# Kernel optimization log

Measured on AMD Instinct MI355X. Metric: run time of the kernel, lower is better.

Reference implementation:

```python
import jax, jax.numpy as jnp
import numpy as np

B, S, D = 1, 4096, 2048
H, KV, HD = 16, 4, 128
GROUPS = H // KV
SCALE = HD ** -0.5
ROPE_BASE = 10000.0
NEG = -1e9


def _rope_tables():
    inv_freq = 1.0 / (ROPE_BASE ** (jnp.arange(0, HD, 2, dtype=jnp.float32) / HD))  # [HD/2]
    pos = jnp.arange(S, dtype=jnp.float32)
    freqs = pos[:, None] * inv_freq[None, :]            # [S, HD/2]
    emb = jnp.concatenate([freqs, freqs], axis=-1)      # [S, HD] (HF convention)
    return jnp.cos(emb)[None], jnp.sin(emb)[None]       # [1, S, HD]


def setup_inputs() -> dict:
    key = jax.random.key(0)
    ks = jax.random.split(key, 6)
    cos, sin = _rope_tables()
    causal = jnp.tril(jnp.ones((S, S), dtype=bool))
    attention_mask = jnp.where(causal, 0.0, NEG).astype(jnp.float32)[None, None]  # [1,1,S,S]
    std = 0.02
    return {
        "hidden_states": jax.random.normal(ks[0], (B, S, D), jnp.float32),
        "cos": cos.astype(jnp.float32),
        "sin": sin.astype(jnp.float32),
        "attention_mask": attention_mask,
        "wq": jax.random.normal(ks[1], (H * HD, D), jnp.float32) * std,
        "wk": jax.random.normal(ks[2], (KV * HD, D), jnp.float32) * std,
        "wv": jax.random.normal(ks[3], (KV * HD, D), jnp.float32) * std,
        "wo": jax.random.normal(ks[4], (D, H * HD), jnp.float32) * std,
    }


def _rotate_half(x):
    x1, x2 = x[..., : HD // 2], x[..., HD // 2:]
    return jnp.concatenate([-x2, x1], axis=-1)


def reference(hidden_states, cos, sin, attention_mask, wq, wk, wv, wo):
    b, s, _ = hidden_states.shape
    # projections -> [B, n_heads, S, HD]
    q = (hidden_states @ wq.T).reshape(b, s, H, HD).transpose(0, 2, 1, 3)
    k = (hidden_states @ wk.T).reshape(b, s, KV, HD).transpose(0, 2, 1, 3)
    v = (hidden_states @ wv.T).reshape(b, s, KV, HD).transpose(0, 2, 1, 3)
    # RoPE (HF apply_rotary_pos_emb, unsqueeze head dim)
    c, sn = cos[:, None], sin[:, None]
    q = q * c + _rotate_half(q) * sn
    k = k * c + _rotate_half(k) * sn
    # GQA: repeat kv heads
    k = jnp.repeat(k, GROUPS, axis=1)
    v = jnp.repeat(v, GROUPS, axis=1)
    # eager attention
    scores = jnp.einsum("bhqd,bhkd->bhqk", q, k) * SCALE + attention_mask
    attn = jax.nn.softmax(scores, axis=-1)
    out = jnp.einsum("bhqk,bhkd->bhqd", attn, v)
    out = out.transpose(0, 2, 1, 3).reshape(b, s, H * HD)
    # output projection (all-reduce is identity at world_size=1)
    return out @ wo.T
```

## Files before the change

### kernel.cpp

```cpp
#include <hip/hip_runtime.h>
#include <hip/hip_bf16.h>

#define SEQ   4096
#define DMODEL 2048
#define NHEAD 16
#define NKVH  4
#define HDIM  128
#define NQ    (NHEAD*HDIM)
#define NKV   (NKVH*HDIM)
#define NQKV  (NQ + 2*NKV)
#define SCALE 0.08838834764831845f
#define LOG2E 1.4426950408889634f
#define SCL2  (SCALE * LOG2E)

typedef __bf16 bf16x4 __attribute__((ext_vector_type(4)));
typedef __bf16 bf16x8 __attribute__((ext_vector_type(8)));
typedef float  f32x4  __attribute__((ext_vector_type(4)));

#define GLOBAL_CPTR(x) ((const __attribute__((address_space(1))) void*)(x))
#define LDS_PTR(x)     ((__attribute__((address_space(3))) void*)(x))

__global__ __launch_bounds__(256)
void convert_all(__bf16* __restrict__ wqkv, __bf16* __restrict__ wob,
                 __bf16* __restrict__ hb,
                 const float* __restrict__ wq, const float* __restrict__ wk,
                 const float* __restrict__ wv, const float* __restrict__ wo,
                 const float* __restrict__ hid)
{
    const int b = blockIdx.x;
    const float* src;
    __bf16* dst;
    int ib;
    if (b < 2048)      { src = wq;  dst = wqkv;                                 ib = b; }
    else if (b < 2560) { src = wk;  dst = wqkv + (size_t)NQ * DMODEL;           ib = b - 2048; }
    else if (b < 3072) { src = wv;  dst = wqkv + (size_t)(NQ + NKV) * DMODEL;   ib = b - 2560; }
    else if (b < 5120) { src = wo;  dst = wob;                                  ib = b - 3072; }
    else               { src = hid; dst = hb;                                   ib = b - 5120; }
    const size_t e0 = ((size_t)ib * 256 + threadIdx.x) * 8;
    const float4 a = *(const float4*)(src + e0);
    const float4 c = *(const float4*)(src + e0 + 4);
    bf16x8 o;
    o[0]=(__bf16)a.x; o[1]=(__bf16)a.y; o[2]=(__bf16)a.z; o[3]=(__bf16)a.w;
    o[4]=(__bf16)c.x; o[5]=(__bf16)c.y; o[6]=(__bf16)c.z; o[7]=(__bf16)c.w;
    *(bf16x8*)(dst + e0) = o;
}

__global__ __launch_bounds__(256)
void gemm_bt(const __bf16* __restrict__ A, const __bf16* __restrict__ Bw,
             void* __restrict__ Cv, __bf16* __restrict__ kb2, __bf16* __restrict__ vt2,
             const float* __restrict__ ct, const float* __restrict__ st,
             int M, int N, int K, int cmode)
{
    __shared__ alignas(16) __bf16 As[2][128*32];
    __shared__ alignas(16) __bf16 Bs[2][128*32];

    const int tid  = threadIdx.x;
    const int w    = tid >> 6;
    const int lane = tid & 63;
    const int l16  = lane & 15;
    const int quad = lane >> 4;
    const int m0 = blockIdx.y * 128;
    const int n0 = blockIdx.x * 128;

    const int srow = lane >> 2;
    const int scol = (((lane & 3) ^ ((lane >> 3) & 3)) * 8);
    const int rsw  = (quad ^ ((l16 >> 1) & 3)) * 8;

    const int wm = (w >> 1) * 64;
    int coff[4];
    #pragma unroll
    for (int nt = 0; nt < 4; ++nt)
        coff[nt] = (cmode == 3) ? ((w & 1) * 32 + ((nt & 2) ? 64 : 0) + (nt & 1) * 16)
                                : ((w & 1) * 64 + nt * 16);

    f32x4 acc[4][4];
    #pragma unroll
    for (int mt = 0; mt < 4; ++mt)
        #pragma unroll
        for (int nt = 0; nt < 4; ++nt)
            acc[mt][nt] = (f32x4){0.f, 0.f, 0.f, 0.f};

    auto STAGE = [&](int k0, int b) {
        #pragma unroll
        for (int c = 0; c < 2; ++c) {
            const int r0 = w * 32 + c * 16;
            const __bf16* ga = A + (size_t)(m0 + r0 + srow) * K + k0 + scol;
            __builtin_amdgcn_global_load_lds(GLOBAL_CPTR(ga), LDS_PTR(&As[b][r0 * 32]), 16, 0, 0);
            const __bf16* gb = Bw + (size_t)(n0 + r0 + srow) * K + k0 + scol;
            __builtin_amdgcn_global_load_lds(GLOBAL_CPTR(gb), LDS_PTR(&Bs[b][r0 * 32]), 16, 0, 0);
        }
    };

    STAGE(0, 0);
    for (int k0 = 0; k0 < K; k0 += 32) {
        const int b = (k0 >> 5) & 1;
        __syncthreads();
        if (k0 + 32 < K) STAGE(k0 + 32, b ^ 1);

        bf16x8 af[4], bf[4];
        #pragma unroll
        for (int mt = 0; mt < 4; ++mt)
            af[mt] = *(const bf16x8*)&As[b][(wm + mt*16 + l16) * 32 + rsw];
        #pragma unroll
        for (int nt = 0; nt < 4; ++nt)
            bf[nt] = *(const bf16x8*)&Bs[b][(coff[nt] + l16) * 32 + rsw];
        __builtin_amdgcn_s_setprio(1);
        #pragma unroll
        for (int mt = 0; mt < 4; ++mt)
            #pragma unroll
            for (int nt = 0; nt < 4; ++nt)
                acc[mt][nt] = __builtin_amdgcn_mfma_f32_16x16x32_bf16(
                    af[mt], bf[nt], acc[mt][nt], 0, 0, 0);
        __builtin_amdgcn_s_setprio(0);
    }

    if (cmode == 3) {
        if (n0 >= 2560) {
            #pragma unroll
            for (int mt = 0; mt < 4; ++mt)
                #pragma unroll
                for (int nt = 0; nt < 4; ++nt) {
                    const int col = (n0 - 2560) + coff[nt] + l16;
                    const int row = m0 + wm + mt*16 + quad*4;
                    bf16x4 pk;
                    #pragma unroll
                    for (int r = 0; r < 4; ++r) pk[r] = (__bf16)acc[mt][nt][r];
                    *(bf16x4*)&vt2[(size_t)col * M + row] = pk;
                }
        } else {
            __bf16* dst;
            int ncols, cb;
            if (n0 < 2048) { dst = (__bf16*)Cv; ncols = NQ;  cb = n0; }
            else           { dst = kb2;         ncols = NKV; cb = n0 - 2048; }
            #pragma unroll
            for (int mt = 0; mt < 4; ++mt)
                #pragma unroll
                for (int np = 0; np < 2; ++np) {
                    const int d = coff[np] + l16;
                    #pragma unroll
                    for (int r = 0; r < 4; ++r) {
                        const int s = m0 + wm + mt*16 + quad*4 + r;
                        const float c  = ct[s * HDIM + d];
                        const float sn = st[s * HDIM + d];
                        const float x1 = acc[mt][np][r];
                        const float x2 = acc[mt][np + 2][r];
                        dst[(size_t)s * ncols + cb + d]      = (__bf16)(x1 * c - x2 * sn);
                        dst[(size_t)s * ncols + cb + d + 64] = (__bf16)(x2 * c + x1 * sn);
                    }
                }
        }
    } else {
        float* Cf = (float*)Cv;
        #pragma unroll
        for (int mt = 0; mt < 4; ++mt)
            #pragma unroll
            for (int nt = 0; nt < 4; ++nt) {
                const int row = m0 + wm + mt*16 + quad*4;
                const int col = n0 + coff[nt] + l16;
                #pragma unroll
                for (int r = 0; r < 4; ++r)
                    Cf[(size_t)(row + r) * N + col] = acc[mt][nt][r];
            }
    }
}

__global__ __launch_bounds__(512, 4)
void attn_kernel(__bf16* __restrict__ QO, const __bf16* __restrict__ Kb,
                 const __bf16* __restrict__ Vt)
{
    __shared__ alignas(16) __bf16 Klds[2][4][64][32];
    __shared__ alignas(16) __bf16 Vlds[2][2][128][32];
    __shared__ alignas(16) __bf16 Ps[8][16][64];

    const int tid  = threadIdx.x;
    const int w    = tid >> 6;
    const int lane = tid & 63;
    const int l16  = lane & 15;
    const int quad = lane >> 4;
    const int bx = (int)blockIdx.x;
    const int h  = (int)blockIdx.y;
    const int g  = h >> 2;
    const int nbx = (int)gridDim.x;
    const int qt = (h < 8) ? (nbx - 1 - bx) : bx;
    const int m0 = qt * 128;
    const int wrow = m0 + w * 16;

    const int srow = lane >> 2;
    const int scol = (((lane & 3) ^ ((lane >> 3) & 3)) * 8);
    const int rsw  = (quad ^ ((l16 >> 1) & 3)) * 8;

    const int kcw = w & 3;
    const int hw  = w >> 2;

    bf16x8 qf[4];
    {
        const size_t qbase = (size_t)(wrow + l16) * NQ + h * HDIM;
        #pragma unroll
        for (int kc = 0; kc < 4; ++kc)
            qf[kc] = *(const bf16x8*)&QO[qbase + kc * 32 + quad * 8];
    }

    bf16x8 onesf;
    #pragma unroll
    for (int i = 0; i < 8; ++i) onesf[i] = (__bf16)1.0f;

    const __bf16* kSrc = Kb + (size_t)(hw * 32 + srow) * NKV + g * HDIM + kcw * 32 + scol;
    const __bf16* vSrc = Vt + (size_t)(g * HDIM + kcw * 32 + srow) * SEQ + hw * 32 + scol;

    auto STAGE = [&](int jj, int b) {
        const int n0g = jj * 64;
        #pragma unroll
        for (int c = 0; c < 2; ++c) {
            __builtin_amdgcn_global_load_lds(
                GLOBAL_CPTR(kSrc + (size_t)(n0g + c * 16) * NKV),
                LDS_PTR(&Klds[b][kcw][hw * 32 + c * 16][0]), 16, 0, 0);
            __builtin_amdgcn_global_load_lds(
                GLOBAL_CPTR(vSrc + (size_t)(c * 16) * SEQ + n0g),
                LDS_PTR(&Vlds[b][hw][kcw * 32 + c * 16][0]), 16, 0, 0);
        }
    };

    f32x4 lacc = (f32x4){0.f, 0.f, 0.f, 0.f};
    f32x4 oacc[8];
    #pragma unroll
    for (int t = 0; t < 8; ++t) oacc[t] = (f32x4){0.f, 0.f, 0.f, 0.f};

    const int njt = 2 * qt + 2;
    STAGE(0, 0);
    for (int j = 0; j < njt; ++j) {
        __syncthreads();
        if (j + 1 < njt) STAGE(j + 1, (j + 1) & 1);
        const int n0g = j * 64;
        if (n0g > wrow + 15) continue;
        const int b = j & 1;

        f32x4 sacc[4];
        #pragma unroll
        for (int nt = 0; nt < 4; ++nt) sacc[nt] = (f32x4){0.f, 0.f, 0.f, 0.f};
        __builtin_amdgcn_s_setprio(1);
        #pragma unroll
        for (int kc = 0; kc < 4; ++kc) {
            #pragma unroll
            for (int nt = 0; nt < 4; ++nt) {
                const bf16x8 kf = *(const bf16x8*)&Klds[b][kc][nt * 16 + l16][rsw];
                sacc[nt] = __builtin_amdgcn_mfma_f32_16x16x32_bf16(qf[kc], kf, sacc[nt], 0, 0, 0);
            }
        }
        __builtin_amdgcn_s_setprio(0);

        if (n0g + 64 > wrow) {
            #pragma unroll
            for (int r = 0; r < 4; ++r) {
                const int qr = wrow + quad * 4 + r;
                const int prow = quad * 4 + r;
                const int pxor = (prow & 7) << 3;
                #pragma unroll
                for (int nt = 0; nt < 4; ++nt) {
                    float e = exp2f(sacc[nt][r] * SCL2);
                    if ((n0g + nt * 16 + l16) > qr) e = 0.f;
                    Ps[w][prow][(nt * 16 + l16) ^ pxor] = (__bf16)e;
                }
            }
        } else {
            #pragma unroll
            for (int r = 0; r < 4; ++r) {
                const int prow = quad * 4 + r;
                const int pxor = (prow & 7) << 3;
                #pragma unroll
                for (int nt = 0; nt < 4; ++nt)
                    Ps[w][prow][(nt * 16 + l16) ^ pxor] = (__bf16)exp2f(sacc[nt][r] * SCL2);
            }
        }

        bf16x8 pa[2];
        #pragma unroll
        for (int kc = 0; kc < 2; ++kc)
            pa[kc] = *(const bf16x8*)&Ps[w][l16][(kc * 32 + quad * 8) ^ ((l16 & 7) << 3)];

        __builtin_amdgcn_s_setprio(1);
        lacc = __builtin_amdgcn_mfma_f32_16x16x32_bf16(pa[0], onesf, lacc, 0, 0, 0);
        lacc = __builtin_amdgcn_mfma_f32_16x16x32_bf16(pa[1], onesf, lacc, 0, 0, 0);
        #pragma unroll
        for (int kc = 0; kc < 2; ++kc)
            #pragma unroll
            for (int t = 0; t < 8; ++t) {
                const bf16x8 vf = *(const bf16x8*)&Vlds[b][kc][t * 16 + l16][rsw];
                oacc[t] = __builtin_amdgcn_mfma_f32_16x16x32_bf16(pa[kc], vf, oacc[t], 0, 0, 0);
            }
        __builtin_amdgcn_s_setprio(0);
    }

    float rinv[4];
    #pragma unroll
    for (int r = 0; r < 4; ++r) rinv[r] = 1.f / lacc[r];
    #pragma unroll
    for (int t = 0; t < 8; ++t)
        #pragma unroll
        for (int r = 0; r < 4; ++r) {
            const int qr = wrow + quad * 4 + r;
            QO[(size_t)qr * NQ + h * HDIM + t * 16 + l16] = (__bf16)(oacc[t][r] * rinv[r]);
        }
}

extern "C" void kernel_launch(void* const* d_in, const int* in_sizes, int n_in,
                              void* d_out, int out_size, void* d_ws, size_t ws_size,
                              hipStream_t stream)
{
    const float* hidden = (const float*)d_in[0];
    const float* cosp   = (const float*)d_in[1];
    const float* sinp   = (const float*)d_in[2];
    const float* wq = (const float*)d_in[4];
    const float* wk = (const float*)d_in[5];
    const float* wv = (const float*)d_in[6];
    const float* wo = (const float*)d_in[7];

    const size_t nw_q = (size_t)NQ  * DMODEL;
    const size_t nw_k = (size_t)NKV * DMODEL;
    const size_t nq_e = (size_t)SEQ * NQ;
    const size_t nk_e = (size_t)SEQ * NKV;

    __bf16* ws     = (__bf16*)d_ws;
    __bf16* wo_b   = ws;
    __bf16* wqkv_b = wo_b + nw_q;
    __bf16* qbuf   = wqkv_b + nw_q + 2 * nw_k;
    __bf16* kbuf   = qbuf + nq_e;
    __bf16* vtb    = kbuf + nk_e;
    __bf16* hbuf   = (__bf16*)d_out;

    convert_all<<<dim3(9216), dim3(256), 0, stream>>>(
        wqkv_b, wo_b, hbuf, wq, wk, wv, wo, hidden);

    gemm_bt<<<dim3(NQKV / 128, SEQ / 128), dim3(256), 0, stream>>>(
        hbuf, wqkv_b, qbuf, kbuf, vtb, cosp, sinp, SEQ, NQKV, DMODEL, 3);

    attn_kernel<<<dim3(SEQ / 128, NHEAD), dim3(512), 0, stream>>>(qbuf, kbuf, vtb);

    gemm_bt<<<dim3(DMODEL / 128, SEQ / 128), dim3(256), 0, stream>>>(
        qbuf, wo_b, d_out, nullptr, nullptr, nullptr, nullptr, SEQ, DMODEL, DMODEL, 1);
}
```

Baseline: 412.7 us.

## Give each attention wave two 16-row query tiles with 256-thread blocks

```diff
diff --git a/kernel.cpp b/kernel.cpp
--- a/kernel.cpp
+++ b/kernel.cpp
@@ -164,13 +164,13 @@
     }
 }
 
-__global__ __launch_bounds__(512, 4)
+__global__ __launch_bounds__(256, 2)
 void attn_kernel(__bf16* __restrict__ QO, const __bf16* __restrict__ Kb,
                  const __bf16* __restrict__ Vt)
 {
     __shared__ alignas(16) __bf16 Klds[2][4][64][32];
     __shared__ alignas(16) __bf16 Vlds[2][2][128][32];
-    __shared__ alignas(16) __bf16 Ps[8][16][64];
+    __shared__ alignas(16) __bf16 Ps[4][32][64];
 
     const int tid  = threadIdx.x;
     const int w    = tid >> 6;
@@ -183,47 +183,49 @@
     const int nbx = (int)gridDim.x;
     const int qt = (h < 8) ? (nbx - 1 - bx) : bx;
     const int m0 = qt * 128;
-    const int wrow = m0 + w * 16;
+    const int wrow = m0 + w * 32;
 
     const int srow = lane >> 2;
     const int scol = (((lane & 3) ^ ((lane >> 3) & 3)) * 8);
     const int rsw  = (quad ^ ((l16 >> 1) & 3)) * 8;
 
-    const int kcw = w & 3;
-    const int hw  = w >> 2;
-
-    bf16x8 qf[4];
-    {
-        const size_t qbase = (size_t)(wrow + l16) * NQ + h * HDIM;
+    bf16x8 qf[2][4];
+    #pragma unroll
+    for (int mt = 0; mt < 2; ++mt) {
+        const size_t qbase = (size_t)(wrow + mt * 16 + l16) * NQ + h * HDIM;
         #pragma unroll
         for (int kc = 0; kc < 4; ++kc)
-            qf[kc] = *(const bf16x8*)&QO[qbase + kc * 32 + quad * 8];
+            qf[mt][kc] = *(const bf16x8*)&QO[qbase + kc * 32 + quad * 8];
     }
 
     bf16x8 onesf;
     #pragma unroll
     for (int i = 0; i < 8; ++i) onesf[i] = (__bf16)1.0f;
 
-    const __bf16* kSrc = Kb + (size_t)(hw * 32 + srow) * NKV + g * HDIM + kcw * 32 + scol;
-    const __bf16* vSrc = Vt + (size_t)(g * HDIM + kcw * 32 + srow) * SEQ + hw * 32 + scol;
+    const __bf16* kSrc = Kb + (size_t)srow * NKV + g * HDIM + w * 32 + scol;
+    const __bf16* vSrc = Vt + (size_t)(g * HDIM + (w >> 1) * 64 + srow) * SEQ + (w & 1) * 32 + scol;
 
     auto STAGE = [&](int jj, int b) {
         const int n0g = jj * 64;
         #pragma unroll
-        for (int c = 0; c < 2; ++c) {
+        for (int c = 0; c < 4; ++c) {
             __builtin_amdgcn_global_load_lds(
                 GLOBAL_CPTR(kSrc + (size_t)(n0g + c * 16) * NKV),
-                LDS_PTR(&Klds[b][kcw][hw * 32 + c * 16][0]), 16, 0, 0);
+                LDS_PTR(&Klds[b][w][c * 16][0]), 16, 0, 0);
             __builtin_amdgcn_global_load_lds(
                 GLOBAL_CPTR(vSrc + (size_t)(c * 16) * SEQ + n0g),
-                LDS_PTR(&Vlds[b][hw][kcw * 32 + c * 16][0]), 16, 0, 0);
+                LDS_PTR(&Vlds[b][w & 1][(w >> 1) * 64 + c * 16][0]), 16, 0, 0);
         }
     };
 
-    f32x4 lacc = (f32x4){0.f, 0.f, 0.f, 0.f};
-    f32x4 oacc[8];
-    #pragma unroll
-    for (int t = 0; t < 8; ++t) oacc[t] = (f32x4){0.f, 0.f, 0.f, 0.f};
+    f32x4 lacc[2];
+    f32x4 oacc[2][8];
+    #pragma unroll
+    for (int mt = 0; mt < 2; ++mt) {
+        lacc[mt] = (f32x4){0.f, 0.f, 0.f, 0.f};
+        #pragma unroll
+        for (int t = 0; t < 8; ++t) oacc[mt][t] = (f32x4){0.f, 0.f, 0.f, 0.f};
+    }
 
     const int njt = 2 * qt + 2;
     STAGE(0, 0);
@@ -231,75 +233,91 @@
         __syncthreads();
         if (j + 1 < njt) STAGE(j + 1, (j + 1) & 1);
         const int n0g = j * 64;
-        if (n0g > wrow + 15) continue;
+        if (n0g > wrow + 31) continue;
         const int b = j & 1;
 
-        f32x4 sacc[4];
-        #pragma unroll
-        for (int nt = 0; nt < 4; ++nt) sacc[nt] = (f32x4){0.f, 0.f, 0.f, 0.f};
+        f32x4 sacc[2][4];
+        #pragma unroll
+        for (int mt = 0; mt < 2; ++mt)
+            #pragma unroll
+            for (int nt = 0; nt < 4; ++nt) sacc[mt][nt] = (f32x4){0.f, 0.f, 0.f, 0.f};
         __builtin_amdgcn_s_setprio(1);
         #pragma unroll
         for (int kc = 0; kc < 4; ++kc) {
             #pragma unroll
             for (int nt = 0; nt < 4; ++nt) {
                 const bf16x8 kf = *(const bf16x8*)&Klds[b][kc][nt * 16 + l16][rsw];
-                sacc[nt] = __builtin_amdgcn_mfma_f32_16x16x32_bf16(qf[kc], kf, sacc[nt], 0, 0, 0);
+                sacc[0][nt] = __builtin_amdgcn_mfma_f32_16x16x32_bf16(qf[0][kc], kf, sacc[0][nt], 0, 0, 0);
+                sacc[1][nt] = __builtin_amdgcn_mfma_f32_16x16x32_bf16(qf[1][kc], kf, sacc[1][nt], 0, 0, 0);
             }
         }
         __builtin_amdgcn_s_setprio(0);
 
-        if (n0g + 64 > wrow) {
-            #pragma unroll
-            for (int r = 0; r < 4; ++r) {
-                const int qr = wrow + quad * 4 + r;
-                const int prow = quad * 4 + r;
-                const int pxor = (prow & 7) << 3;
-                #pragma unroll
-                for (int nt = 0; nt < 4; ++nt) {
-                    float e = exp2f(sacc[nt][r] * SCL2);
-                    if ((n0g + nt * 16 + l16) > qr) e = 0.f;
-                    Ps[w][prow][(nt * 16 + l16) ^ pxor] = (__bf16)e;
+        #pragma unroll
+        for (int mt = 0; mt < 2; ++mt) {
+            const int rowbase = wrow + mt * 16;
+            if (n0g + 64 > rowbase) {
+                #pragma unroll
+                for (int r = 0; r < 4; ++r) {
+                    const int qr = rowbase + quad * 4 + r;
+                    const int prow = mt * 16 + quad * 4 + r;
+                    const int pxor = (prow & 7) << 3;
+                    #pragma unroll
+                    for (int nt = 0; nt < 4; ++nt) {
+                        float e = exp2f(sacc[mt][nt][r] * SCL2);
+                        if ((n0g + nt * 16 + l16) > qr) e = 0.f;
+                        Ps[w][prow][(nt * 16 + l16) ^ pxor] = (__bf16)e;
+                    }
                 }
-            }
-        } else {
-            #pragma unroll
-            for (int r = 0; r < 4; ++r) {
-                const int prow = quad * 4 + r;
-                const int pxor = (prow & 7) << 3;
-                #pragma unroll
-                for (int nt = 0; nt < 4; ++nt)
-                    Ps[w][prow][(nt * 16 + l16) ^ pxor] = (__bf16)exp2f(sacc[nt][r] * SCL2);
-            }
-        }
-
-        bf16x8 pa[2];
-        #pragma unroll
-        for (int kc = 0; kc < 2; ++kc)
-            pa[kc] = *(const bf16x8*)&Ps[w][l16][(kc * 32 + quad * 8) ^ ((l16 & 7) << 3)];
+            } else {
+                #pragma unroll
+                for (int r = 0; r < 4; ++r) {
+                    const int prow = mt * 16 + quad * 4 + r;
+                    const int pxor = (prow & 7) << 3;
+                    #pragma unroll
+                    for (int nt = 0; nt < 4; ++nt)
+                        Ps[w][prow][(nt * 16 + l16) ^ pxor] = (__bf16)exp2f(sacc[mt][nt][r] * SCL2);
+                }
+            }
+        }
+
+        bf16x8 pa[2][2];
+        #pragma unroll
+        for (int mt = 0; mt < 2; ++mt)
+            #pragma unroll
+            for (int kc = 0; kc < 2; ++kc)
+                pa[mt][kc] = *(const bf16x8*)&Ps[w][mt * 16 + l16][(kc * 32 + quad * 8) ^ ((l16 & 7) << 3)];
 
         __builtin_amdgcn_s_setprio(1);
-        lacc = __builtin_amdgcn_mfma_f32_16x16x32_bf16(pa[0], onesf, lacc, 0, 0, 0);
-        lacc = __builtin_amdgcn_mfma_f32_16x16x32_bf16(pa[1], onesf, lacc, 0, 0, 0);
+        #pragma unroll
+        for (int mt = 0; mt < 2; ++mt) {
+            lacc[mt] = __builtin_amdgcn_mfma_f32_16x16x32_bf16(pa[mt][0], onesf, lacc[mt], 0, 0, 0);
+            lacc[mt] = __builtin_amdgcn_mfma_f32_16x16x32_bf16(pa[mt][1], onesf, lacc[mt], 0, 0, 0);
+        }
         #pragma unroll
         for (int kc = 0; kc < 2; ++kc)
             #pragma unroll
             for (int t = 0; t < 8; ++t) {
                 const bf16x8 vf = *(const bf16x8*)&Vlds[b][kc][t * 16 + l16][rsw];
-                oacc[t] = __builtin_amdgcn_mfma_f32_16x16x32_bf16(pa[kc], vf, oacc[t], 0, 0, 0);
+                oacc[0][t] = __builtin_amdgcn_mfma_f32_16x16x32_bf16(pa[0][kc], vf, oacc[0][t], 0, 0, 0);
+                oacc[1][t] = __builtin_amdgcn_mfma_f32_16x16x32_bf16(pa[1][kc], vf, oacc[1][t], 0, 0, 0);
             }
         __builtin_amdgcn_s_setprio(0);
     }
 
-    float rinv[4];
-    #pragma unroll
-    for (int r = 0; r < 4; ++r) rinv[r] = 1.f / lacc[r];
-    #pragma unroll
-    for (int t = 0; t < 8; ++t)
-        #pragma unroll
-        for (int r = 0; r < 4; ++r) {
-            const int qr = wrow + quad * 4 + r;
-            QO[(size_t)qr * NQ + h * HDIM + t * 16 + l16] = (__bf16)(oacc[t][r] * rinv[r]);
-        }
+    #pragma unroll
+    for (int mt = 0; mt < 2; ++mt) {
+        float rinv[4];
+        #pragma unroll
+        for (int r = 0; r < 4; ++r) rinv[r] = 1.f / lacc[mt][r];
+        #pragma unroll
+        for (int t = 0; t < 8; ++t)
+            #pragma unroll
+            for (int r = 0; r < 4; ++r) {
+                const int qr = wrow + mt * 16 + quad * 4 + r;
+                QO[(size_t)qr * NQ + h * HDIM + t * 16 + l16] = (__bf16)(oacc[mt][t][r] * rinv[r]);
+            }
+    }
 }
 
 extern "C" void kernel_launch(void* const* d_in, const int* in_sizes, int n_in,
@@ -333,7 +351,7 @@
     gemm_bt<<<dim3(NQKV / 128, SEQ / 128), dim3(256), 0, stream>>>(
         hbuf, wqkv_b, qbuf, kbuf, vtb, cosp, sinp, SEQ, NQKV, DMODEL, 3);
 
-    attn_kernel<<<dim3(SEQ / 128, NHEAD), dim3(512), 0, stream>>>(qbuf, kbuf, vtb);
+    attn_kernel<<<dim3(SEQ / 128, NHEAD), dim3(256), 0, stream>>>(qbuf, kbuf, vtb);
 
     gemm_bt<<<dim3(DMODEL / 128, SEQ / 128), dim3(256), 0, stream>>>(
         qbuf, wo_b, d_out, nullptr, nullptr, nullptr, nullptr, SEQ, DMODEL, DMODEL, 1);
```

After: 436.1 us. +5.7%, slower.
